# Performance work log

Hardware: AMD Instinct MI355X
Metric: run time of the kernel (lower is better)

The kernel has to match this reference:

```python
import jax, jax.numpy as jnp
import numpy as np

B, N, C = 4, 1024, 1024
H = 16
HD = C // H
FF = 4 * C
EPS = 1e-6


def layernorm(x, g, b):
    mu = jnp.mean(x, axis=-1, keepdims=True)
    var = jnp.mean((x - mu) ** 2, axis=-1, keepdims=True)
    return (x - mu) * jax.lax.rsqrt(var + EPS) * g + b


def setup_inputs() -> dict:
    key = jax.random.key(0)
    ks = jax.random.split(key, 16)
    s = lambda fan_in: 1.0 / np.sqrt(fan_in)
    inp = {
        "x": jax.random.normal(ks[0], (B, N, C), dtype=jnp.float32),
        "qkv_w": jax.random.normal(ks[1], (3 * C, C), dtype=jnp.float32) * s(C),
        "qkv_b": jnp.zeros((3 * C,), jnp.float32),
        "attn_proj_w": jax.random.normal(ks[2], (C, C), dtype=jnp.float32) * s(C),
        "attn_proj_b": jnp.zeros((C,), jnp.float32),
        "blk_proj_w": jax.random.normal(ks[3], (C, C), dtype=jnp.float32) * s(C),
        "blk_proj_b": jnp.zeros((C,), jnp.float32),
        "ln1_g": jnp.ones((C,), jnp.float32),
        "ln1_b": jnp.zeros((C,), jnp.float32),
        "ln2_g": jnp.ones((C,), jnp.float32),
        "ln2_b": jnp.zeros((C,), jnp.float32),
        "fc1_w": jax.random.normal(ks[4], (FF, C), dtype=jnp.float32) * s(C),
        "fc1_b": jnp.zeros((FF,), jnp.float32),
        "fc2_w": jax.random.normal(ks[5], (C, FF), dtype=jnp.float32) * s(FF),
        "fc2_b": jnp.zeros((C,), jnp.float32),
        "mask": jnp.ones((B, N), jnp.int32),  # unused by the original forward
    }
    return inp


def reference(x, qkv_w, qkv_b, attn_proj_w, attn_proj_b, blk_proj_w, blk_proj_b,
              ln1_g, ln1_b, ln2_g, ln2_b, fc1_w, fc1_b, fc2_w, fc2_b, mask):
    shortcut = x
    xn = layernorm(x, ln1_g, ln1_b)

    # QKV projection: [B,N,3C] -> [3,B,H,N,HD]
    qkv = xn @ qkv_w.T + qkv_b
    qkv = qkv.reshape(B, N, 3, H, HD).transpose(2, 0, 3, 1, 4)
    q, k, v = qkv[0], qkv[1], qkv[2]
    scale = HD ** -0.5
    attn = jnp.einsum('bhqd,bhkd->bhqk', q * scale, k)
    attn = jax.nn.softmax(attn, axis=-1)
    o = jnp.einsum('bhqk,bhkd->bhqd', attn, v)
    o = o.transpose(0, 2, 1, 3).reshape(B, N, C)
    o = o @ attn_proj_w.T + attn_proj_b  # attention-internal proj

    x = shortcut + (o @ blk_proj_w.T + blk_proj_b)  # Block's extra proj + residual

    h = layernorm(x, ln2_g, ln2_b)
    h = jax.nn.gelu(h @ fc1_w.T + fc1_b, approximate=False)
    h = h @ fc2_w.T + fc2_b
    return x + h
```

## Files before the change

### kernel.cpp

```cpp
#include <hip/hip_runtime.h>

typedef unsigned short u16;
typedef __attribute__((ext_vector_type(8))) short short8;
typedef __attribute__((ext_vector_type(4))) float f32x4;

#define DEVI __device__ __forceinline__

static constexpr int Nn = 1024;
static constexpr int Cc = 1024;

DEVI u16 f2bf(float f) {
  union { float f; unsigned u; } v; v.f = f;
  unsigned r = v.u + 0x7fffu + ((v.u >> 16) & 1u);
  return (u16)(r >> 16);
}

DEVI void async_ld16(const void* g, void* lds) {
  __builtin_amdgcn_global_load_lds(
      (__attribute__((address_space(1))) void*)g,
      (__attribute__((address_space(3))) void*)lds, 16, 0, 0);
}

__global__ __launch_bounds__(256) void prep_k(
    const float* __restrict__ s0, const float* __restrict__ s2,
    const float* __restrict__ s3, const float* __restrict__ s4,
    u16* __restrict__ out,
    const float* __restrict__ apw, u16* __restrict__ wapT,
    const float* __restrict__ apb, const float* __restrict__ bpw,
    const float* __restrict__ bpb, float* __restrict__ cb) {
  __shared__ u16 tile[64][72];
  const int B = blockIdx.x;
  if (B < 12288) {
    const size_t j = ((size_t)B * 256 + threadIdx.x) * 4;
    size_t i; const float* src; size_t lo;
    if (j < 3145728) { i = j; src = s0; lo = 0; }
    else {
      i = j + 1048576;
      if (i < 5242880)      { src = s2; lo = 4194304; }
      else if (i < 9437184) { src = s3; lo = 5242880; }
      else                  { src = s4; lo = 9437184; }
    }
    const float4 v = *(const float4*)&src[i - lo];
    ushort4 o;
    o.x = f2bf(v.x); o.y = f2bf(v.y); o.z = f2bf(v.z); o.w = f2bf(v.w);
    *(ushort4*)&out[i] = o;
  } else if (B < 12544) {
    const int bb = B - 12288;
    const int bx = bb & 15, by = bb >> 4;
    const int tr = threadIdx.x >> 2;
    const int tc4 = (threadIdx.x & 3) * 16;
#pragma unroll
    for (int j = 0; j < 4; ++j) {
      const float4 v = *(const float4*)&apw[(size_t)(by * 64 + tr) * 1024 +
                                            bx * 64 + tc4 + j * 4];
      tile[tc4 + j * 4 + 0][tr] = f2bf(v.x);
      tile[tc4 + j * 4 + 1][tr] = f2bf(v.y);
      tile[tc4 + j * 4 + 2][tr] = f2bf(v.z);
      tile[tc4 + j * 4 + 3][tr] = f2bf(v.w);
    }
    __syncthreads();
#pragma unroll
    for (int j = 0; j < 4; ++j) {
      ushort4 o;
      o.x = tile[tr][tc4 + j * 4 + 0];
      o.y = tile[tr][tc4 + j * 4 + 1];
      o.z = tile[tr][tc4 + j * 4 + 2];
      o.w = tile[tr][tc4 + j * 4 + 3];
      *(ushort4*)&wapT[(size_t)(bx * 64 + tr) * 1024 + by * 64 + tc4 + j * 4] = o;
    }
  } else {
    const int bb = B - 12544;
    const int j = bb * 4 + (threadIdx.x >> 6);
    const int lane = threadIdx.x & 63;
    float s = 0.f;
    for (int k = lane; k < 1024; k += 64) s += apb[k] * bpw[(size_t)j * 1024 + k];
#pragma unroll
    for (int m = 1; m < 64; m <<= 1) s += __shfl_xor(s, m);
    if (lane == 0) cb[j] = s + bpb[j];
  }
}

__global__ __launch_bounds__(256) void g64ln(
    const u16* __restrict__ A, const u16* __restrict__ W,
    u16* __restrict__ wc,
    const float* __restrict__ x, const float* __restrict__ gg,
    const float* __restrict__ bb, u16* __restrict__ xn) {
  __shared__ __align__(16) u16 As[64 * 64];
  __shared__ __align__(16) u16 Bs[64 * 64];
  __shared__ float ps[4], ps2[4];
  const int tid = threadIdx.x;
  if (blockIdx.x < 256) {
    const int wave = tid >> 6, lane = tid & 63;
    const int g = lane >> 4, lr = lane & 15;
    const int brow = (blockIdx.x >> 4) << 6, bcol = (blockIdx.x & 15) << 6;
    const int srow = lane >> 3;
    const int scg = (lane & 7) ^ srow;
    const int swz = (lr & 7) << 4;

    f32x4 acc[4];
#pragma unroll
    for (int j = 0; j < 4; ++j) acc[j] = (f32x4){0.f, 0.f, 0.f, 0.f};

    for (int k0 = 0; k0 < 1024; k0 += 64) {
#pragma unroll
      for (int u = 0; u < 2; ++u) {
        async_ld16(A + (size_t)(brow + u * 32 + wave * 8 + srow) * 1024 + k0 + scg * 8,
                   (char*)As + u * 4096 + wave * 1024);
        async_ld16(W + (size_t)(bcol + u * 32 + wave * 8 + srow) * 1024 + k0 + scg * 8,
                   (char*)Bs + u * 4096 + wave * 1024);
      }
      __syncthreads();
      short8 af[2], bf[4][2];
#pragma unroll
      for (int kk = 0; kk < 2; ++kk)
        af[kk] = *(const short8*)((char*)As + (wave * 16 + lr) * 128 +
                                  ((kk * 64 + g * 16) ^ swz));
#pragma unroll
      for (int nf = 0; nf < 4; ++nf)
#pragma unroll
        for (int kk = 0; kk < 2; ++kk)
          bf[nf][kk] = *(const short8*)((char*)Bs + (nf * 16 + lr) * 128 +
                                        ((kk * 64 + g * 16) ^ swz));
#pragma unroll
      for (int kk = 0; kk < 2; ++kk)
#pragma unroll
        for (int nf = 0; nf < 4; ++nf)
          acc[nf] = __builtin_amdgcn_mfma_f32_16x16x32_bf16(af[kk], bf[nf][kk],
                                                            acc[nf], 0, 0, 0);
      __syncthreads();
    }
#pragma unroll
    for (int nf = 0; nf < 4; ++nf)
#pragma unroll
      for (int reg = 0; reg < 4; ++reg)
        wc[(size_t)(brow + wave * 16 + g * 4 + reg) * 1024 +
           bcol + nf * 16 + lr] = f2bf(acc[nf][reg]);
  } else {
    const int row = blockIdx.x - 256;
    const float4 v = ((const float4*)(x + (size_t)row * 1024))[tid];
    float s  = v.x + v.y + v.z + v.w;
    float s2 = v.x * v.x + v.y * v.y + v.z * v.z + v.w * v.w;
#pragma unroll
    for (int m = 1; m < 64; m <<= 1) { s += __shfl_xor(s, m); s2 += __shfl_xor(s2, m); }
    const int wave = tid >> 6;
    if ((tid & 63) == 0) { ps[wave] = s; ps2[wave] = s2; }
    __syncthreads();
    s = ps[0] + ps[1] + ps[2] + ps[3];
    s2 = ps2[0] + ps2[1] + ps2[2] + ps2[3];
    const float mu = s * (1.0f / 1024.0f);
    const float var = s2 * (1.0f / 1024.0f) - mu * mu;
    const float rs = rsqrtf(var + 1e-6f);
    const float4 gv = ((const float4*)gg)[tid];
    const float4 bv = ((const float4*)bb)[tid];
    ushort4 o;
    o.x = f2bf((v.x - mu) * rs * gv.x + bv.x);
    o.y = f2bf((v.y - mu) * rs * gv.y + bv.y);
    o.z = f2bf((v.z - mu) * rs * gv.z + bv.z);
    o.w = f2bf((v.w - mu) * rs * gv.w + bv.w);
    ((ushort4*)(xn + (size_t)row * 1024))[tid] = o;
  }
}

__global__ __launch_bounds__(256) void ln_bf16(const float* __restrict__ x,
                                               const float* __restrict__ gg,
                                               const float* __restrict__ bb,
                                               u16* __restrict__ out) {
  const int row = blockIdx.x;
  const float4 v = ((const float4*)(x + (size_t)row * 1024))[threadIdx.x];
  float s  = v.x + v.y + v.z + v.w;
  float s2 = v.x * v.x + v.y * v.y + v.z * v.z + v.w * v.w;
#pragma unroll
  for (int m = 1; m < 64; m <<= 1) { s += __shfl_xor(s, m); s2 += __shfl_xor(s2, m); }
  __shared__ float ps[4], ps2[4];
  const int wave = threadIdx.x >> 6;
  if ((threadIdx.x & 63) == 0) { ps[wave] = s; ps2[wave] = s2; }
  __syncthreads();
  s = ps[0] + ps[1] + ps[2] + ps[3];
  s2 = ps2[0] + ps2[1] + ps2[2] + ps2[3];
  const float mu = s * (1.0f / 1024.0f);
  const float var = s2 * (1.0f / 1024.0f) - mu * mu;
  const float rs = rsqrtf(var + 1e-6f);
  const float4 gv = ((const float4*)gg)[threadIdx.x];
  const float4 bv = ((const float4*)bb)[threadIdx.x];
  ushort4 o;
  o.x = f2bf((v.x - mu) * rs * gv.x + bv.x);
  o.y = f2bf((v.y - mu) * rs * gv.y + bv.y);
  o.z = f2bf((v.z - mu) * rs * gv.z + bv.z);
  o.w = f2bf((v.w - mu) * rs * gv.w + bv.w);
  ((ushort4*)(out + (size_t)row * 1024))[threadIdx.x] = o;
}

template <bool GELU_, bool OUTBF>
__global__ __launch_bounds__(512, 4) void gemmS(
    const u16* __restrict__ A, const u16* __restrict__ W,
    const float* __restrict__ bias, void* __restrict__ out,
    int M, int N, int K) {
  __shared__ __align__(16) u16 As[256 * 64];
  __shared__ __align__(16) u16 Bs[128 * 64];
  const int tid = threadIdx.x;
  const int wave = tid >> 6, lane = tid & 63;
  const int g = lane >> 4, lr = lane & 15;
  const int wm = wave >> 1, wn = wave & 1;
  const int ntile = N >> 7;
  const int nwg = gridDim.x;
  int bid = blockIdx.x;
  bid = (bid & 7) * (nwg >> 3) + (bid >> 3);
  const int brow = (bid / ntile) << 8, bcol = (bid % ntile) << 7;

  const int sru = wave * 8 + (lane >> 3);
  const int scg = (lane & 7) ^ (lane >> 3);
  const int swz = (lr & 7) << 4;

  f32x4 acc[4][4];
#pragma unroll
  for (int i = 0; i < 4; ++i)
#pragma unroll
    for (int j = 0; j < 4; ++j) acc[i][j] = (f32x4){0.f, 0.f, 0.f, 0.f};

  for (int k0 = 0; k0 < K; k0 += 64) {
#pragma unroll
    for (int u = 0; u < 2; ++u)
      async_ld16(W + (size_t)(bcol + u * 64 + sru) * K + k0 + scg * 8,
                 (char*)Bs + u * 8192 + wave * 1024);
#pragma unroll
    for (int u = 0; u < 4; ++u)
      async_ld16(A + (size_t)(brow + u * 64 + sru) * K + k0 + scg * 8,
                 (char*)As + u * 8192 + wave * 1024);
    asm volatile("s_waitcnt vmcnt(0)" ::: "memory");
    __builtin_amdgcn_s_barrier();

    short8 bf[4][2];
#pragma unroll
    for (int nf = 0; nf < 4; ++nf) {
      const int row = wn * 64 + nf * 16 + lr;
#pragma unroll
      for (int kk = 0; kk < 2; ++kk)
        bf[nf][kk] = *(const short8*)((const char*)Bs + row * 128 +
                                      ((kk * 64 + g * 16) ^ swz));
    }
    __builtin_amdgcn_s_setprio(1);
#pragma unroll
    for (int mf = 0; mf < 4; ++mf) {
      short8 af[2];
      const int row = wm * 64 + mf * 16 + lr;
#pragma unroll
      for (int kk = 0; kk < 2; ++kk)
        af[kk] = *(const short8*)((const char*)As + row * 128 +
                                  ((kk * 64 + g * 16) ^ swz));
#pragma unroll
      for (int nf = 0; nf < 4; ++nf)
#pragma unroll
        for (int kk = 0; kk < 2; ++kk)
          acc[mf][nf] = __builtin_amdgcn_mfma_f32_16x16x32_bf16(
              af[kk], bf[nf][kk], acc[mf][nf], 0, 0, 0);
    }
    __builtin_amdgcn_s_setprio(0);
    __builtin_amdgcn_s_barrier();
  }

#pragma unroll
  for (int mf = 0; mf < 4; ++mf)
#pragma unroll
    for (int nf = 0; nf < 4; ++nf) {
      const int cI = bcol + wn * 64 + nf * 16 + lr;
      const float bv = bias[cI];
#pragma unroll
      for (int reg = 0; reg < 4; ++reg) {
        const int r = brow + wm * 64 + mf * 16 + g * 4 + reg;
        float v = acc[mf][nf][reg] + bv;
        if (GELU_) v = 0.5f * v * (1.0f + erff(v * 0.70710678118654752f));
        if (OUTBF) ((u16*)out)[(size_t)r * N + cI] = f2bf(v);
        else       ((float*)out)[(size_t)r * N + cI] = v;
      }
    }
}

__global__ __launch_bounds__(512, 4) void gemmS96(
    const u16* __restrict__ A, const u16* __restrict__ W,
    const float* __restrict__ bias, u16* __restrict__ out,
    u16* __restrict__ vt, int M, int N, int K) {
  __shared__ __align__(16) u16 As[256 * 64];
  __shared__ __align__(16) u16 Bs[96 * 64];
  const int tid = threadIdx.x;
  const int wave = tid >> 6, lane = tid & 63;
  const int g = lane >> 4, lr = lane & 15;
  const int wm = wave >> 1, wn = wave & 1;
  const int ntile = N / 96;
  const int nwg = gridDim.x;
  int bid = blockIdx.x;
  bid = (bid & 7) * (nwg >> 3) + (bid >> 3);
  const int brow = (bid / ntile) << 8;
  const int bcol = (bid % ntile) * 96;

  const int sru = wave * 8 + (lane >> 3);
  const int scg = (lane & 7) ^ (lane >> 3);
  const int swz = (lr & 7) << 4;
  const int brG = tid >> 3;
  const int bcg = (tid & 7) ^ (brG & 7);

  f32x4 acc[4][3];
#pragma unroll
  for (int i = 0; i < 4; ++i)
#pragma unroll
    for (int j = 0; j < 3; ++j) acc[i][j] = (f32x4){0.f, 0.f, 0.f, 0.f};

  for (int k0 = 0; k0 < K; k0 += 64) {
    async_ld16(W + (size_t)(bcol + brG) * K + k0 + bcg * 8,
               (char*)Bs + tid * 16);
    if (wave < 4)
      async_ld16(W + (size_t)(bcol + 64 + brG) * K + k0 + bcg * 8,
                 (char*)Bs + 8192 + tid * 16);
#pragma unroll
    for (int u = 0; u < 4; ++u)
      async_ld16(A + (size_t)(brow + u * 64 + sru) * K + k0 + scg * 8,
                 (char*)As + u * 8192 + wave * 1024);
    asm volatile("s_waitcnt vmcnt(0)" ::: "memory");
    __builtin_amdgcn_s_barrier();

    short8 bf[3][2];
#pragma unroll
    for (int nf = 0; nf < 3; ++nf) {
      const int row = wn * 48 + nf * 16 + lr;
#pragma unroll
      for (int kk = 0; kk < 2; ++kk)
        bf[nf][kk] = *(const short8*)((const char*)Bs + row * 128 +
                                      ((kk * 64 + g * 16) ^ swz));
    }
    __builtin_amdgcn_s_setprio(1);
#pragma unroll
    for (int mf = 0; mf < 4; ++mf) {
      short8 af[2];
      const int row = wm * 64 + mf * 16 + lr;
#pragma unroll
      for (int kk = 0; kk < 2; ++kk)
        af[kk] = *(const short8*)((const char*)As + row * 128 +
                                  ((kk * 64 + g * 16) ^ swz));
#pragma unroll
      for (int nf = 0; nf < 3; ++nf)
#pragma unroll
        for (int kk = 0; kk < 2; ++kk)
          acc[mf][nf] = __builtin_amdgcn_mfma_f32_16x16x32_bf16(
              af[kk], bf[nf][kk], acc[mf][nf], 0, 0, 0);
    }
    __builtin_amdgcn_s_setprio(0);
    __builtin_amdgcn_s_barrier();
  }

#pragma unroll
  for (int nf = 0; nf < 3; ++nf) {
    const int cb0 = bcol + wn * 48 + nf * 16;
    const int cI = cb0 + lr;
    const float bv = bias[cI];
    if (cb0 < 2048) {
#pragma unroll
      for (int mf = 0; mf < 4; ++mf)
#pragma unroll
        for (int reg = 0; reg < 4; ++reg) {
          const int r = brow + wm * 64 + mf * 16 + g * 4 + reg;
          out[(size_t)r * N + cI] = f2bf(acc[mf][nf][reg] + bv);
        }
    } else {
      const int dg0 = cb0 - 2048;
      const int hh = dg0 >> 6;
      const int d = (dg0 & 63) + lr;
#pragma unroll
      for (int mf = 0; mf < 4; ++mf)
#pragma unroll
        for (int reg = 0; reg < 4; ++reg) {
          const int r = brow + wm * 64 + mf * 16 + g * 4 + reg;
          const int b = r >> 10, t = r & 1023;
          vt[(size_t)(((b << 4) + hh) * 64 + d) * 1024 + t] =
              f2bf(acc[mf][nf][reg] + bv);
        }
    }
  }
}

template <bool GELU_, bool RESID, bool OUTBF>
__global__ __launch_bounds__(512, 2) void gemm128t(
    const u16* __restrict__ A, const u16* __restrict__ W,
    const float* __restrict__ bias, const float* __restrict__ resid,
    void* __restrict__ out, int M, int N, int K) {
  __shared__ __align__(16) u16 smem[49152];
  const int tid = threadIdx.x;
  const int wave = tid >> 6, lane = tid & 63;
  const int g = lane >> 4, lr = lane & 15;
  const int kg = wave & 1, ws = wave >> 1;
  const int wm = ws >> 1, wn = ws & 1;
  const int ntile = N >> 7;
  const int nwg = gridDim.x;
  int bid = blockIdx.x;
  bid = (bid & 7) * (nwg >> 3) + (bid >> 3);
  const int brow = (bid / ntile) << 7, bcol = (bid % ntile) << 7;

  const int sru = wave * 8 + (lane >> 3);
  const int scg = (lane & 7) ^ (lane >> 3);
  const int NT = K >> 6;

  f32x4 acc[4][4];
#pragma unroll
  for (int i = 0; i < 4; ++i)
#pragma unroll
    for (int j = 0; j < 4; ++j) acc[i][j] = (f32x4){0.f, 0.f, 0.f, 0.f};

  auto STAGE = [&](int b, int kt) {
    char* base = (char*)smem + b * 32768;
#pragma unroll
    for (int u = 0; u < 2; ++u)
      async_ld16(W + (size_t)(bcol + u * 64 + sru) * K + (size_t)kt * 64 + scg * 8,
                 base + 16384 + u * 8192 + wave * 1024);
#pragma unroll
    for (int u = 0; u < 2; ++u)
      async_ld16(A + (size_t)(brow + u * 64 + sru) * K + (size_t)kt * 64 + scg * 8,
                 base + u * 8192 + wave * 1024);
  };

  const int colb = kg * 64 + g * 16;
  const int swz = (lr & 7) << 4;

  STAGE(0, 0);
  STAGE(1, 1 < NT ? 1 : 0);
  asm volatile("s_waitcnt vmcnt(4)" ::: "memory");
  __builtin_amdgcn_s_barrier();

  for (int t = 0; t < NT; ++t) {
    const int b = t % 3;
    const char* Ab = (const char*)smem + b * 32768;
    const char* Bb = Ab + 16384;

    short8 bf[4], af[4];
#pragma unroll
    for (int nf = 0; nf < 4; ++nf)
      bf[nf] = *(const short8*)(Bb + (wn * 64 + nf * 16 + lr) * 128 +
                                (colb ^ swz));
#pragma unroll
    for (int mf = 0; mf < 2; ++mf) {
      af[mf]     = *(const short8*)(Ab + (wm * 32 + mf * 16 + lr) * 128 +
                                    (colb ^ swz));
      af[mf + 2] = *(const short8*)(Ab + (64 + wm * 32 + mf * 16 + lr) * 128 +
                                    (colb ^ swz));
    }
    {
      const int pt = (t + 2 < NT) ? t + 2 : NT - 1;
      STAGE((t + 2) % 3, pt);
    }
    __builtin_amdgcn_s_setprio(1);
#pragma unroll
    for (int mf = 0; mf < 4; ++mf)
#pragma unroll
      for (int nf = 0; nf < 4; ++nf)
        acc[mf][nf] = __builtin_amdgcn_mfma_f32_16x16x32_bf16(
            af[mf], bf[nf], acc[mf][nf], 0, 0, 0);
    __builtin_amdgcn_s_setprio(0);
    asm volatile("s_waitcnt vmcnt(4)" ::: "memory");
    __builtin_amdgcn_s_barrier();
  }

  asm volatile("s_waitcnt vmcnt(0)" ::: "memory");
  __syncthreads();
  float* pr = (float*)smem + (size_t)((wm << 1) | wn) * 4096;
  if (kg == 1) {
#pragma unroll
    for (int mf = 0; mf < 4; ++mf)
#pragma unroll
      for (int nf = 0; nf < 4; ++nf)
#pragma unroll
        for (int reg = 0; reg < 4; ++reg) {
          const int lrow = mf * 16 + g * 4 + reg;
          const int w = lrow * 64 +
                        ((nf * 16 + lr) ^ (g << 2) ^ ((g & 1) << 4));
          pr[w] = acc[mf][nf][reg];
        }
  }
  __syncthreads();
  if (kg == 0) {
#pragma unroll
    for (int mf = 0; mf < 4; ++mf) {
      const int rb = brow + ((mf < 2) ? wm * 32 + mf * 16
                                      : 64 + wm * 32 + (mf - 2) * 16);
#pragma unroll
      for (int nf = 0; nf < 4; ++nf) {
        const int cI = bcol + wn * 64 + nf * 16 + lr;
        const float bv = bias[cI];
#pragma unroll
        for (int reg = 0; reg < 4; ++reg) {
          const int lrow = mf * 16 + g * 4 + reg;
          const int w = lrow * 64 +
                        ((nf * 16 + lr) ^ (g << 2) ^ ((g & 1) << 4));
          const int r = rb + g * 4 + reg;
          float v = acc[mf][nf][reg] + pr[w] + bv;
          if (GELU_) v = 0.5f * v * (1.0f + erff(v * 0.70710678118654752f));
          if (RESID) v += resid[(size_t)r * N + cI];
          if (OUTBF) ((u16*)out)[(size_t)r * N + cI] = f2bf(v);
          else       ((float*)out)[(size_t)r * N + cI] = v;
        }
      }
    }
  }
}

__global__ __launch_bounds__(512) void attn_kernel(const u16* __restrict__ qkv,
                                                   const u16* __restrict__ vt,
                                                   u16* __restrict__ o_out) {
  const int D = blockIdx.x;
  const int bh = (D & 7) + 8 * (D >> 6);
  const int qb = (D >> 3) & 7;
  const int b = bh >> 4, h = bh & 15;
  const int tid = threadIdx.x, wave = tid >> 6, lane = tid & 63;
  const int g = lane >> 4, lr = lane & 15;
  const u16* qg = qkv + (size_t)b * Nn * 3072 + h * 64;
  const u16* kg = qg + 1024;
  const u16* vgt = vt + (size_t)bh * 64 * 1024;

  __shared__ __align__(16) u16 Kl[64 * 64];
  __shared__ __align__(16) u16 Vt[64 * 64];
  __shared__ __align__(16) u16 Pl[128 * 64];

  const int q0 = qb * 128 + wave * 16;
  short8 qf[2];
#pragma unroll
  for (int kf = 0; kf < 2; ++kf)
    qf[kf] = *(const short8*)(qg + (size_t)(q0 + lr) * 3072 + kf * 32 + g * 8);

  f32x4 o[4];
  float ll[4];
#pragma unroll
  for (int df = 0; df < 4; ++df) o[df] = (f32x4){0.f, 0.f, 0.f, 0.f};
#pragma unroll
  for (int r = 0; r < 4; ++r) ll[r] = 0.f;

  const int sc = wave * 64 + lane;
  const int st = sc >> 3;
  const int sob = ((sc & 7) << 4) ^ ((st & 7) << 4);

  for (int t0 = 0; t0 < Nn; t0 += 64) {
    async_ld16(kg + (size_t)(t0 + st) * 3072 + (sob >> 1),
               (char*)Kl + (size_t)(wave * 64) * 16);
    async_ld16(vgt + (size_t)st * 1024 + t0 + (sob >> 1),
               (char*)Vt + (size_t)(wave * 64) * 16);
    __syncthreads();

    short8 kfr[4][2];
#pragma unroll
    for (int tf = 0; tf < 4; ++tf) {
      const int t = tf * 16 + lr;
#pragma unroll
      for (int kf = 0; kf < 2; ++kf)
        kfr[tf][kf] = *(const short8*)((const char*)Kl + t * 128 +
                                       ((kf * 64 + g * 16) ^ ((t & 7) << 4)));
    }
    f32x4 s[4];
    __builtin_amdgcn_s_setprio(1);
#pragma unroll
    for (int tf = 0; tf < 4; ++tf) {
      f32x4 z = (f32x4){0.f, 0.f, 0.f, 0.f};
      z = __builtin_amdgcn_mfma_f32_16x16x32_bf16(qf[0], kfr[tf][0], z, 0, 0, 0);
      z = __builtin_amdgcn_mfma_f32_16x16x32_bf16(qf[1], kfr[tf][1], z, 0, 0, 0);
      s[tf] = z;
    }
    __builtin_amdgcn_s_setprio(0);

    short8 vfr[4][2];
#pragma unroll
    for (int df = 0; df < 4; ++df) {
      const int d = df * 16 + lr;
#pragma unroll
      for (int kf = 0; kf < 2; ++kf)
        vfr[df][kf] = *(const short8*)((const char*)Vt + d * 128 +
                                       ((kf * 64 + g * 16) ^ ((d & 7) << 4)));
    }

#pragma unroll
    for (int tf = 0; tf < 4; ++tf)
#pragma unroll
      for (int reg = 0; reg < 4; ++reg) {
        const float p = __expf(s[tf][reg] * 0.125f);
        s[tf][reg] = p;
        ll[reg] += p;
      }

#pragma unroll
    for (int tf = 0; tf < 4; ++tf)
#pragma unroll
      for (int reg = 0; reg < 4; ++reg) {
        const int m = wave * 16 + g * 4 + reg;
        const int t2 = (tf * 16 + lr) * 2;
        *(u16*)((char*)Pl + m * 128 + (t2 ^ ((m & 7) << 4))) = f2bf(s[tf][reg]);
      }
    short8 pa[2];
#pragma unroll
    for (int kf = 0; kf < 2; ++kf)
      pa[kf] = *(const short8*)((const char*)Pl + (wave * 16 + lr) * 128 +
                                ((kf * 64 + g * 16) ^ ((lr & 7) << 4)));
    __builtin_amdgcn_s_setprio(1);
#pragma unroll
    for (int df = 0; df < 4; ++df) {
      o[df] = __builtin_amdgcn_mfma_f32_16x16x32_bf16(pa[0], vfr[df][0], o[df], 0, 0, 0);
      o[df] = __builtin_amdgcn_mfma_f32_16x16x32_bf16(pa[1], vfr[df][1], o[df], 0, 0, 0);
    }
    __builtin_amdgcn_s_setprio(0);
    __syncthreads();
  }

#pragma unroll
  for (int reg = 0; reg < 4; ++reg) {
#pragma unroll
    for (int msk = 1; msk < 16; msk <<= 1) ll[reg] += __shfl_xor(ll[reg], msk);
    const float inv = 1.0f / ll[reg];
    const int row = b * Nn + qb * 128 + wave * 16 + g * 4 + reg;
#pragma unroll
    for (int df = 0; df < 4; ++df) {
      const int col = h * 64 + df * 16 + lr;
      o_out[(size_t)row * 1024 + col] = f2bf(o[df][reg] * inv);
    }
  }
}

extern "C" void kernel_launch(void* const* d_in, const int* in_sizes, int n_in,
                              void* d_out, int out_size, void* d_ws, size_t ws_size,
                              hipStream_t stream) {
  const float* x    = (const float*)d_in[0];
  const float* qkvw = (const float*)d_in[1];
  const float* qkvb = (const float*)d_in[2];
  const float* apw  = (const float*)d_in[3];
  const float* apb  = (const float*)d_in[4];
  const float* bpw  = (const float*)d_in[5];
  const float* bpb  = (const float*)d_in[6];
  const float* ln1g = (const float*)d_in[7];
  const float* ln1b = (const float*)d_in[8];
  const float* ln2g = (const float*)d_in[9];
  const float* ln2b = (const float*)d_in[10];
  const float* fc1w = (const float*)d_in[11];
  const float* fc1b = (const float*)d_in[12];
  const float* fc2w = (const float*)d_in[13];
  const float* fc2b = (const float*)d_in[14];
  float* out = (float*)d_out;

  char* ws = (char*)d_ws;
  size_t off = 0;
  auto alloc = [&](size_t bytes) {
    char* p = ws + off;
    off += (bytes + 255) & ~(size_t)255;
    return p;
  };
  u16* wqkv  = (u16*)alloc((size_t)3145728 * 2);
  u16* wap   = (u16*)alloc((size_t)1048576 * 2);
  u16* wbp   = (u16*)alloc((size_t)1048576 * 2);
  u16* wfc1  = (u16*)alloc((size_t)4194304 * 2);
  u16* wfc2  = (u16*)alloc((size_t)4194304 * 2);
  u16* xn    = (u16*)alloc((size_t)4194304 * 2);
  u16* qkvbf = (u16*)alloc((size_t)12582912 * 2);
  u16* obuf  = (u16*)alloc((size_t)4194304 * 2);
  float* x2  = (float*)alloc((size_t)4194304 * 4);
  u16* wapT  = (u16*)alloc((size_t)1048576 * 2);
  u16* wc    = (u16*)alloc((size_t)1048576 * 2);
  float* cb  = (float*)alloc(1024 * 4);
  u16* vt    = (u16*)alloc((size_t)4194304 * 2);
  u16* ff    = qkvbf;
  (void)wap;

  prep_k<<<12800, 256, 0, stream>>>(qkvw, bpw, fc1w, fc2w, wqkv,
                                    apw, wapT, apb, bpw, bpb, cb);

  g64ln<<<4352, 256, 0, stream>>>(wbp, wapT, wc, x, ln1g, ln1b, xn);

  gemmS96<<<512, 512, 0, stream>>>(
      xn, wqkv, qkvb, qkvbf, vt, 4096, 3072, 1024);

  attn_kernel<<<512, 512, 0, stream>>>(qkvbf, vt, obuf);

  gemm128t<false, true, false><<<256, 512, 0, stream>>>(
      obuf, wc, cb, x, x2, 4096, 1024, 1024);

  ln_bf16<<<4096, 256, 0, stream>>>(x2, ln2g, ln2b, xn);

  gemmS<true, true><<<512, 512, 0, stream>>>(
      xn, wfc1, fc1b, ff, 4096, 4096, 1024);

  gemm128t<false, true, false><<<256, 512, 0, stream>>>(
      ff, wfc2, fc2b, x2, out, 4096, 1024, 4096);
}
```

Before: 207.2 us.

## Merge LN1 into prep kernel and wc GEMM into QKV kernel launch

Moves the layernorm-1 row blocks into the weight-prep kernel and folds the small blk_proj×attn_proj weight-combining GEMM into the QKV GEMM launch as extra blocks. This removes one kernel launch and lets the small GEMM run alongside the large QKV GEMM instead of serialising before it. In exchange, the extra blocks use 512-thread workgroups where only 4 waves compute, and they carry the larger shared-memory footprint of the QKV kernel.

```diff
diff --git a/kernel.cpp b/kernel.cpp
--- a/kernel.cpp
+++ b/kernel.cpp
@@ -27,11 +27,15 @@
     u16* __restrict__ out,
     const float* __restrict__ apw, u16* __restrict__ wapT,
     const float* __restrict__ apb, const float* __restrict__ bpw,
-    const float* __restrict__ bpb, float* __restrict__ cb) {
+    const float* __restrict__ bpb, float* __restrict__ cb,
+    const float* __restrict__ x, const float* __restrict__ ln1g,
+    const float* __restrict__ ln1b, u16* __restrict__ xn) {
   __shared__ u16 tile[64][72];
+  __shared__ float ps[4], ps2[4];
   const int B = blockIdx.x;
+  const int tid = threadIdx.x;
   if (B < 12288) {
-    const size_t j = ((size_t)B * 256 + threadIdx.x) * 4;
+    const size_t j = ((size_t)B * 256 + tid) * 4;
     size_t i; const float* src; size_t lo;
     if (j < 3145728) { i = j; src = s0; lo = 0; }
     else {
@@ -47,8 +51,8 @@
   } else if (B < 12544) {
     const int bb = B - 12288;
     const int bx = bb & 15, by = bb >> 4;
-    const int tr = threadIdx.x >> 2;
-    const int tc4 = (threadIdx.x & 3) * 16;
+    const int tr = tid >> 2;
+    const int tc4 = (tid & 3) * 16;
 #pragma unroll
     for (int j = 0; j < 4; ++j) {
       const float4 v = *(const float4*)&apw[(size_t)(by * 64 + tr) * 1024 +
@@ -68,75 +72,17 @@
       o.w = tile[tr][tc4 + j * 4 + 3];
       *(ushort4*)&wapT[(size_t)(bx * 64 + tr) * 1024 + by * 64 + tc4 + j * 4] = o;
     }
-  } else {
+  } else if (B < 12800) {
     const int bb = B - 12544;
-    const int j = bb * 4 + (threadIdx.x >> 6);
-    const int lane = threadIdx.x & 63;
+    const int j = bb * 4 + (tid >> 6);
+    const int lane = tid & 63;
     float s = 0.f;
     for (int k = lane; k < 1024; k += 64) s += apb[k] * bpw[(size_t)j * 1024 + k];
 #pragma unroll
     for (int m = 1; m < 64; m <<= 1) s += __shfl_xor(s, m);
     if (lane == 0) cb[j] = s + bpb[j];
-  }
-}
-
-__global__ __launch_bounds__(256) void g64ln(
-    const u16* __restrict__ A, const u16* __restrict__ W,
-    u16* __restrict__ wc,
-    const float* __restrict__ x, const float* __restrict__ gg,
-    const float* __restrict__ bb, u16* __restrict__ xn) {
-  __shared__ __align__(16) u16 As[64 * 64];
-  __shared__ __align__(16) u16 Bs[64 * 64];
-  __shared__ float ps[4], ps2[4];
-  const int tid = threadIdx.x;
-  if (blockIdx.x < 256) {
-    const int wave = tid >> 6, lane = tid & 63;
-    const int g = lane >> 4, lr = lane & 15;
-    const int brow = (blockIdx.x >> 4) << 6, bcol = (blockIdx.x & 15) << 6;
-    const int srow = lane >> 3;
-    const int scg = (lane & 7) ^ srow;
-    const int swz = (lr & 7) << 4;
-
-    f32x4 acc[4];
-#pragma unroll
-    for (int j = 0; j < 4; ++j) acc[j] = (f32x4){0.f, 0.f, 0.f, 0.f};
-
-    for (int k0 = 0; k0 < 1024; k0 += 64) {
-#pragma unroll
-      for (int u = 0; u < 2; ++u) {
-        async_ld16(A + (size_t)(brow + u * 32 + wave * 8 + srow) * 1024 + k0 + scg * 8,
-                   (char*)As + u * 4096 + wave * 1024);
-        async_ld16(W + (size_t)(bcol + u * 32 + wave * 8 + srow) * 1024 + k0 + scg * 8,
-                   (char*)Bs + u * 4096 + wave * 1024);
-      }
-      __syncthreads();
-      short8 af[2], bf[4][2];
-#pragma unroll
-      for (int kk = 0; kk < 2; ++kk)
-        af[kk] = *(const short8*)((char*)As + (wave * 16 + lr) * 128 +
-                                  ((kk * 64 + g * 16) ^ swz));
-#pragma unroll
-      for (int nf = 0; nf < 4; ++nf)
-#pragma unroll
-        for (int kk = 0; kk < 2; ++kk)
-          bf[nf][kk] = *(const short8*)((char*)Bs + (nf * 16 + lr) * 128 +
-                                        ((kk * 64 + g * 16) ^ swz));
-#pragma unroll
-      for (int kk = 0; kk < 2; ++kk)
-#pragma unroll
-        for (int nf = 0; nf < 4; ++nf)
-          acc[nf] = __builtin_amdgcn_mfma_f32_16x16x32_bf16(af[kk], bf[nf][kk],
-                                                            acc[nf], 0, 0, 0);
-      __syncthreads();
-    }
-#pragma unroll
-    for (int nf = 0; nf < 4; ++nf)
-#pragma unroll
-      for (int reg = 0; reg < 4; ++reg)
-        wc[(size_t)(brow + wave * 16 + g * 4 + reg) * 1024 +
-           bcol + nf * 16 + lr] = f2bf(acc[nf][reg]);
   } else {
-    const int row = blockIdx.x - 256;
+    const int row = B - 12800;
     const float4 v = ((const float4*)(x + (size_t)row * 1024))[tid];
     float s  = v.x + v.y + v.z + v.w;
     float s2 = v.x * v.x + v.y * v.y + v.z * v.z + v.w * v.w;
@@ -150,8 +96,8 @@
     const float mu = s * (1.0f / 1024.0f);
     const float var = s2 * (1.0f / 1024.0f) - mu * mu;
     const float rs = rsqrtf(var + 1e-6f);
-    const float4 gv = ((const float4*)gg)[tid];
-    const float4 bv = ((const float4*)bb)[tid];
+    const float4 gv = ((const float4*)ln1g)[tid];
+    const float4 bv = ((const float4*)ln1b)[tid];
     ushort4 o;
     o.x = f2bf((v.x - mu) * rs * gv.x + bv.x);
     o.y = f2bf((v.y - mu) * rs * gv.y + bv.y);
@@ -275,103 +221,160 @@
     }
 }
 
-__global__ __launch_bounds__(512, 4) void gemmS96(
+__global__ __launch_bounds__(512, 4) void qkv_k(
     const u16* __restrict__ A, const u16* __restrict__ W,
     const float* __restrict__ bias, u16* __restrict__ out,
-    u16* __restrict__ vt, int M, int N, int K) {
+    u16* __restrict__ vt,
+    const u16* __restrict__ wbp, const u16* __restrict__ wapT,
+    u16* __restrict__ wc) {
   __shared__ __align__(16) u16 As[256 * 64];
   __shared__ __align__(16) u16 Bs[96 * 64];
   const int tid = threadIdx.x;
   const int wave = tid >> 6, lane = tid & 63;
   const int g = lane >> 4, lr = lane & 15;
-  const int wm = wave >> 1, wn = wave & 1;
-  const int ntile = N / 96;
-  const int nwg = gridDim.x;
-  int bid = blockIdx.x;
-  bid = (bid & 7) * (nwg >> 3) + (bid >> 3);
-  const int brow = (bid / ntile) << 8;
-  const int bcol = (bid % ntile) * 96;
-
-  const int sru = wave * 8 + (lane >> 3);
-  const int scg = (lane & 7) ^ (lane >> 3);
   const int swz = (lr & 7) << 4;
-  const int brG = tid >> 3;
-  const int bcg = (tid & 7) ^ (brG & 7);
-
-  f32x4 acc[4][3];
-#pragma unroll
-  for (int i = 0; i < 4; ++i)
-#pragma unroll
-    for (int j = 0; j < 3; ++j) acc[i][j] = (f32x4){0.f, 0.f, 0.f, 0.f};
-
-  for (int k0 = 0; k0 < K; k0 += 64) {
-    async_ld16(W + (size_t)(bcol + brG) * K + k0 + bcg * 8,
-               (char*)Bs + tid * 16);
-    if (wave < 4)
-      async_ld16(W + (size_t)(bcol + 64 + brG) * K + k0 + bcg * 8,
-                 (char*)Bs + 8192 + tid * 16);
-#pragma unroll
-    for (int u = 0; u < 4; ++u)
-      async_ld16(A + (size_t)(brow + u * 64 + sru) * K + k0 + scg * 8,
-                 (char*)As + u * 8192 + wave * 1024);
-    asm volatile("s_waitcnt vmcnt(0)" ::: "memory");
-    __builtin_amdgcn_s_barrier();
-
-    short8 bf[3][2];
+  const int M = 4096, N = 3072, K = 1024;
+
+  if (blockIdx.x < 512) {
+    const int wm = wave >> 1, wn = wave & 1;
+    const int ntile = N / 96;
+    int bid = blockIdx.x;
+    bid = (bid & 7) * 64 + (bid >> 3);
+    const int brow = (bid / ntile) << 8;
+    const int bcol = (bid % ntile) * 96;
+
+    const int sru = wave * 8 + (lane >> 3);
+    const int scg = (lane & 7) ^ (lane >> 3);
+    const int brG = tid >> 3;
+    const int bcg = (tid & 7) ^ (brG & 7);
+
+    f32x4 acc[4][3];
+#pragma unroll
+    for (int i = 0; i < 4; ++i)
+#pragma unroll
+      for (int j = 0; j < 3; ++j) acc[i][j] = (f32x4){0.f, 0.f, 0.f, 0.f};
+
+    for (int k0 = 0; k0 < K; k0 += 64) {
+      async_ld16(W + (size_t)(bcol + brG) * K + k0 + bcg * 8,
+                 (char*)Bs + tid * 16);
+      if (wave < 4)
+        async_ld16(W + (size_t)(bcol + 64 + brG) * K + k0 + bcg * 8,
+                   (char*)Bs + 8192 + tid * 16);
+#pragma unroll
+      for (int u = 0; u < 4; ++u)
+        async_ld16(A + (size_t)(brow + u * 64 + sru) * K + k0 + scg * 8,
+                   (char*)As + u * 8192 + wave * 1024);
+      asm volatile("s_waitcnt vmcnt(0)" ::: "memory");
+      __builtin_amdgcn_s_barrier();
+
+      short8 bf[3][2];
+#pragma unroll
+      for (int nf = 0; nf < 3; ++nf) {
+        const int row = wn * 48 + nf * 16 + lr;
+#pragma unroll
+        for (int kk = 0; kk < 2; ++kk)
+          bf[nf][kk] = *(const short8*)((const char*)Bs + row * 128 +
+                                        ((kk * 64 + g * 16) ^ swz));
+      }
+      __builtin_amdgcn_s_setprio(1);
+#pragma unroll
+      for (int mf = 0; mf < 4; ++mf) {
+        short8 af[2];
+        const int row = wm * 64 + mf * 16 + lr;
+#pragma unroll
+        for (int kk = 0; kk < 2; ++kk)
+          af[kk] = *(const short8*)((const char*)As + row * 128 +
+                                    ((kk * 64 + g * 16) ^ swz));
+#pragma unroll
+        for (int nf = 0; nf < 3; ++nf)
+#pragma unroll
+          for (int kk = 0; kk < 2; ++kk)
+            acc[mf][nf] = __builtin_amdgcn_mfma_f32_16x16x32_bf16(
+                af[kk], bf[nf][kk], acc[mf][nf], 0, 0, 0);
+      }
+      __builtin_amdgcn_s_setprio(0);
+      __builtin_amdgcn_s_barrier();
+    }
+
 #pragma unroll
     for (int nf = 0; nf < 3; ++nf) {
-      const int row = wn * 48 + nf * 16 + lr;
-#pragma unroll
-      for (int kk = 0; kk < 2; ++kk)
-        bf[nf][kk] = *(const short8*)((const char*)Bs + row * 128 +
-                                      ((kk * 64 + g * 16) ^ swz));
-    }
-    __builtin_amdgcn_s_setprio(1);
-#pragma unroll
-    for (int mf = 0; mf < 4; ++mf) {
-      short8 af[2];
-      const int row = wm * 64 + mf * 16 + lr;
-#pragma unroll
-      for (int kk = 0; kk < 2; ++kk)
-        af[kk] = *(const short8*)((const char*)As + row * 128 +
-                                  ((kk * 64 + g * 16) ^ swz));
-#pragma unroll
-      for (int nf = 0; nf < 3; ++nf)
+      const int cb0 = bcol + wn * 48 + nf * 16;
+      const int cI = cb0 + lr;
+      const float bv = bias[cI];
+      if (cb0 < 2048) {
+#pragma unroll
+        for (int mf = 0; mf < 4; ++mf)
+#pragma unroll
+          for (int reg = 0; reg < 4; ++reg) {
+            const int r = brow + wm * 64 + mf * 16 + g * 4 + reg;
+            out[(size_t)r * N + cI] = f2bf(acc[mf][nf][reg] + bv);
+          }
+      } else {
+        const int dg0 = cb0 - 2048;
+        const int hh = dg0 >> 6;
+        const int d = (dg0 & 63) + lr;
+#pragma unroll
+        for (int mf = 0; mf < 4; ++mf)
+#pragma unroll
+          for (int reg = 0; reg < 4; ++reg) {
+            const int r = brow + wm * 64 + mf * 16 + g * 4 + reg;
+            const int b = r >> 10, t = r & 1023;
+            vt[(size_t)(((b << 4) + hh) * 64 + d) * 1024 + t] =
+                f2bf(acc[mf][nf][reg] + bv);
+          }
+      }
+    }
+  } else {
+    const int bb = blockIdx.x - 512;
+    const int brow = (bb >> 4) << 6, bcol = (bb & 15) << 6;
+    const int srow = lane >> 3;
+    const int scg = (lane & 7) ^ srow;
+    const bool act = wave < 4;
+
+    f32x4 acc[4];
+#pragma unroll
+    for (int j = 0; j < 4; ++j) acc[j] = (f32x4){0.f, 0.f, 0.f, 0.f};
+
+    for (int k0 = 0; k0 < 1024; k0 += 64) {
+      if (act) {
+#pragma unroll
+        for (int u = 0; u < 2; ++u) {
+          async_ld16(wbp + (size_t)(brow + u * 32 + wave * 8 + srow) * 1024 + k0 + scg * 8,
+                     (char*)As + u * 4096 + wave * 1024);
+          async_ld16(wapT + (size_t)(bcol + u * 32 + wave * 8 + srow) * 1024 + k0 + scg * 8,
+                     (char*)Bs + u * 4096 + wave * 1024);
+        }
+      }
+      asm volatile("s_waitcnt vmcnt(0)" ::: "memory");
+      __builtin_amdgcn_s_barrier();
+      if (act) {
+        short8 af[2], bf[4][2];
 #pragma unroll
         for (int kk = 0; kk < 2; ++kk)
-          acc[mf][nf] = __builtin_amdgcn_mfma_f32_16x16x32_bf16(
-              af[kk], bf[nf][kk], acc[mf][nf], 0, 0, 0);
-    }
-    __builtin_amdgcn_s_setprio(0);
-    __builtin_amdgcn_s_barrier();
-  }
-
-#pragma unroll
-  for (int nf = 0; nf < 3; ++nf) {
-    const int cb0 = bcol + wn * 48 + nf * 16;
-    const int cI = cb0 + lr;
-    const float bv = bias[cI];
-    if (cb0 < 2048) {
-#pragma unroll
-      for (int mf = 0; mf < 4; ++mf)
-#pragma unroll
-        for (int reg = 0; reg < 4; ++reg) {
-          const int r = brow + wm * 64 + mf * 16 + g * 4 + reg;
-          out[(size_t)r * N + cI] = f2bf(acc[mf][nf][reg] + bv);
-        }
-    } else {
-      const int dg0 = cb0 - 2048;
-      const int hh = dg0 >> 6;
-      const int d = (dg0 & 63) + lr;
-#pragma unroll
-      for (int mf = 0; mf < 4; ++mf)
-#pragma unroll
-        for (int reg = 0; reg < 4; ++reg) {
-          const int r = brow + wm * 64 + mf * 16 + g * 4 + reg;
-          const int b = r >> 10, t = r & 1023;
-          vt[(size_t)(((b << 4) + hh) * 64 + d) * 1024 + t] =
-              f2bf(acc[mf][nf][reg] + bv);
-        }
+          af[kk] = *(const short8*)((char*)As + (wave * 16 + lr) * 128 +
+                                    ((kk * 64 + g * 16) ^ swz));
+#pragma unroll
+        for (int nf = 0; nf < 4; ++nf)
+#pragma unroll
+          for (int kk = 0; kk < 2; ++kk)
+            bf[nf][kk] = *(const short8*)((char*)Bs + (nf * 16 + lr) * 128 +
+                                          ((kk * 64 + g * 16) ^ swz));
+#pragma unroll
+        for (int kk = 0; kk < 2; ++kk)
+#pragma unroll
+          for (int nf = 0; nf < 4; ++nf)
+            acc[nf] = __builtin_amdgcn_mfma_f32_16x16x32_bf16(af[kk], bf[nf][kk],
+                                                              acc[nf], 0, 0, 0);
+      }
+      __builtin_amdgcn_s_barrier();
+    }
+    if (act) {
+#pragma unroll
+      for (int nf = 0; nf < 4; ++nf)
+#pragma unroll
+        for (int reg = 0; reg < 4; ++reg)
+          wc[(size_t)(brow + wave * 16 + g * 4 + reg) * 1024 +
+             bcol + nf * 16 + lr] = f2bf(acc[nf][reg]);
     }
   }
 }
@@ -659,13 +662,11 @@
   u16* ff    = qkvbf;
   (void)wap;
 
-  prep_k<<<12800, 256, 0, stream>>>(qkvw, bpw, fc1w, fc2w, wqkv,
-                                    apw, wapT, apb, bpw, bpb, cb);
-
-  g64ln<<<4352, 256, 0, stream>>>(wbp, wapT, wc, x, ln1g, ln1b, xn);
-
-  gemmS96<<<512, 512, 0, stream>>>(
-      xn, wqkv, qkvb, qkvbf, vt, 4096, 3072, 1024);
+  prep_k<<<16896, 256, 0, stream>>>(qkvw, bpw, fc1w, fc2w, wqkv,
+                                    apw, wapT, apb, bpw, bpb, cb,
+                                    x, ln1g, ln1b, xn);
+
+  qkv_k<<<768, 512, 0, stream>>>(xn, wqkv, qkvb, qkvbf, vt, wbp, wapT, wc);
 
   attn_kernel<<<512, 512, 0, stream>>>(qkvbf, vt, obuf);
 
```

Result: no change. 203.2 us (-1.9%).
